# Performance work log

Hardware: AMD Instinct MI355X
Metric: run time of the kernel (lower is better)

Reference implementation:

```python
import jax, jax.numpy as jnp
import numpy as np


def gcn_conv(x, W, b, edge_index, n_nodes):
    """PyG GCNConv: symmetric-normalized aggregation with self-loops.
    out[j] = sum_{(i->j)} deg(i)^-1/2 deg(j)^-1/2 * (x @ W)[i] + b
    """
    xl = x @ W  # [N, H]
    loop = jnp.arange(n_nodes)
    src = jnp.concatenate([edge_index[0], loop])
    dst = jnp.concatenate([edge_index[1], loop])
    deg = jax.ops.segment_sum(jnp.ones_like(dst, dtype=xl.dtype), dst, num_segments=n_nodes)
    dinv = jax.lax.rsqrt(deg)  # deg >= 1 due to self-loops
    norm = dinv[src] * dinv[dst]  # [E+N]
    msg = xl[src] * norm[:, None]  # [E+N, H]
    return jax.ops.segment_sum(msg, dst, num_segments=n_nodes) + b


def reference(x, edge_index_I, edge_index_D, edge_label_index, W_conv, b_conv, W1, b1, W2, b2):
    n = x.shape[0]
    # encode: shared conv over both graphs, relu, sum (dropout off: eval mode)
    h_I = jax.nn.relu(gcn_conv(x, W_conv, b_conv, edge_index_I, n))
    h_D = jax.nn.relu(gcn_conv(x, W_conv, b_conv, edge_index_D, n))
    z = h_I + h_D  # [N, H]
    # decode: gather endpoints, concat [zi, zj, |zi-zj|], small MLP -> scalar per pair
    zi = z[edge_label_index[0]]  # [P, H]
    zj = z[edge_label_index[1]]  # [P, H]
    pair = jnp.concatenate([zi, zj, jnp.abs(zi - zj)], axis=1)  # [P, 3H]
    hdn = jax.nn.relu(pair @ W1 + b1)
    return jnp.squeeze(hdn @ W2 + b2, axis=-1)  # [P]


def setup_inputs() -> dict:
    key = jax.random.key(0)
    ks = jax.random.split(key, 8)
    N, F, H, E, P = 50000, 256, 128, 800000, 500000
    return {
        "x": jax.random.normal(ks[0], (N, F), dtype=jnp.float32),
        "edge_index_I": jax.random.randint(ks[1], (2, E), 0, N, dtype=jnp.int64),
        "edge_index_D": jax.random.randint(ks[2], (2, E), 0, N, dtype=jnp.int64),
        "edge_label_index": jax.random.randint(ks[3], (2, P), 0, N, dtype=jnp.int64),
        "W_conv": jax.random.normal(ks[4], (F, H), dtype=jnp.float32) * (1.0 / np.sqrt(F)),
        "b_conv": jnp.zeros((H,), dtype=jnp.float32),
        "W1": jax.random.normal(ks[5], (3 * H, H), dtype=jnp.float32) * (1.0 / np.sqrt(3 * H)),
        "b1": jnp.zeros((H,), dtype=jnp.float32),
        "W2": jax.random.normal(ks[6], (H, 1), dtype=jnp.float32) * (1.0 / np.sqrt(H)),
        "b2": jnp.zeros((1,), dtype=jnp.float32),
    }
```

## Files before the change

### kernel.cpp

```cpp
#include <hip/hip_runtime.h>

typedef short short8 __attribute__((ext_vector_type(8)));
typedef float f32x4 __attribute__((ext_vector_type(4)));
typedef float f32x16 __attribute__((ext_vector_type(16)));
typedef unsigned short ushort_t;
typedef unsigned int uint_t;

#define HD __device__ __forceinline__

HD ushort_t f2bf(float f) {
    uint_t u = __float_as_uint(f);
    uint_t r = (u + 0x7fffu + ((u >> 16) & 1u)) >> 16;
    return (ushort_t)r;
}
HD float bf2f(ushort_t h) { return __uint_as_float(((uint_t)h) << 16); }
HD float readlane_f(float v, int l) {
    return __int_as_float(__builtin_amdgcn_readlane(__float_as_int(v), l));
}

__global__ __launch_bounds__(256) void gemm_mfma_hilo_bf16(
    const float* __restrict__ A, const ushort_t* __restrict__ Bth,
    const ushort_t* __restrict__ Btl, ushort_t* __restrict__ C,
    int M, int K, int Ntot) {
    __shared__ ushort_t Ah[128][72], Al[128][72], Bh[128][72], Bl[128][72];
    int tid = threadIdx.x;
    int lane = tid & 63, w = tid >> 6;
    int row0 = blockIdx.x * 128;
    int col0 = blockIdx.y * 128;
    int cl = lane & 31, hi = lane >> 5;
    f32x16 acc[4] = {};
    for (int k0 = 0; k0 < K; k0 += 64) {
        for (int e = tid; e < 4096; e += 256) {
            int r = e >> 5, k2 = e & 31;
            int gr = row0 + r;
            float2 v = {0.f, 0.f};
            if (gr < M) v = *(const float2*)&A[(long)gr * K + k0 + k2 * 2];
            ushort_t h0 = f2bf(v.x); ushort_t l0 = f2bf(v.x - bf2f(h0));
            ushort_t h1 = f2bf(v.y); ushort_t l1 = f2bf(v.y - bf2f(h1));
            *(uint_t*)&Ah[r][k2 * 2] = (uint_t)h0 | ((uint_t)h1 << 16);
            *(uint_t*)&Al[r][k2 * 2] = (uint_t)l0 | ((uint_t)l1 << 16);
        }
        for (int e = tid; e < 4096; e += 256) {
            int n = e >> 5, k2 = e & 31;
            const uint_t* ph = (const uint_t*)&Bth[(long)(col0 + n) * K + k0];
            const uint_t* pl = (const uint_t*)&Btl[(long)(col0 + n) * K + k0];
            *(uint_t*)&Bh[n][k2 * 2] = ph[k2];
            *(uint_t*)&Bl[n][k2 * 2] = pl[k2];
        }
        __syncthreads();
        int arow = w * 32 + cl;
#pragma unroll
        for (int kk = 0; kk < 4; ++kk) {
            int koff = kk * 16 + hi * 8;
            short8 a_h = *(const short8*)&Ah[arow][koff];
            short8 a_l = *(const short8*)&Al[arow][koff];
#pragma unroll
            for (int nf = 0; nf < 4; ++nf) {
                int bcol = nf * 32 + cl;
                short8 b_h = *(const short8*)&Bh[bcol][koff];
                short8 b_l = *(const short8*)&Bl[bcol][koff];
                acc[nf] = __builtin_amdgcn_mfma_f32_32x32x16_bf16(a_h, b_h, acc[nf], 0, 0, 0);
                acc[nf] = __builtin_amdgcn_mfma_f32_32x32x16_bf16(a_l, b_h, acc[nf], 0, 0, 0);
                acc[nf] = __builtin_amdgcn_mfma_f32_32x32x16_bf16(a_h, b_l, acc[nf], 0, 0, 0);
            }
        }
        __syncthreads();
    }
#pragma unroll
    for (int nf = 0; nf < 4; ++nf) {
#pragma unroll
        for (int reg = 0; reg < 16; ++reg) {
            int crow = (reg & 3) + 8 * (reg >> 2) + 4 * hi + w * 32;
            int gr = row0 + crow;
            if (gr < M) C[(long)gr * Ntot + col0 + nf * 32 + cl] = f2bf(acc[nf][reg]);
        }
    }
}

__global__ void prep_bt_conv(const float* __restrict__ Wc, ushort_t* bh, ushort_t* bl) {
    int idx = blockIdx.x * 256 + threadIdx.x;
    if (idx >= 128 * 256) return;
    int n = idx >> 8, k = idx & 255;
    float v = Wc[k * 128 + n];
    ushort_t h = f2bf(v);
    bh[idx] = h;
    bl[idx] = f2bf(v - bf2f(h));
}

__global__ void prep_w1frag(const float* __restrict__ W1, ushort_t* __restrict__ w1f) {
    int idx = blockIdx.x * 256 + threadIdx.x;
    if (idx >= 3 * 16384) return;
    int m = idx >> 14;
    int rem = idx & 16383;
    int f = rem >> 9, l = (rem >> 3) & 63, e = rem & 7;
    int t = f >> 2, kk = f & 3;
    int col = 16 * t + (l & 15);
    int k = kk * 32 + (l >> 4) * 8 + e;
    w1f[idx] = f2bf(W1[(m * 128 + k) * 128 + col]);
}

__global__ void zero_ints(int* p, int n) {
    int i = blockIdx.x * 256 + threadIdx.x;
    if (i < n) p[i] = 0;
}

__global__ void count_deg(const int* __restrict__ dstI, const int* __restrict__ dstD,
                          int* cnt, int N, int E) {
    int e = blockIdx.x * 256 + threadIdx.x;
    if (e < E) {
        atomicAdd(&cnt[dstI[e]], 1);
        atomicAdd(&cnt[N + dstD[e]], 1);
    }
}

__global__ void scan_partial(const int* __restrict__ cnt, int* partials, int n2) {
    __shared__ int sdata[256];
    int i = blockIdx.x * 256 + threadIdx.x;
    sdata[threadIdx.x] = (i < n2) ? cnt[i] : 0;
    __syncthreads();
    for (int s = 128; s > 0; s >>= 1) {
        if (threadIdx.x < s) sdata[threadIdx.x] += sdata[threadIdx.x + s];
        __syncthreads();
    }
    if (threadIdx.x == 0) partials[blockIdx.x] = sdata[0];
}

__global__ void scan_partials_excl2(int* partials, int nb) {
    __shared__ int sd[512];
    int t = threadIdx.x;
    int v = (t < nb) ? partials[t] : 0;
    sd[t] = v;
    __syncthreads();
    for (int s = 1; s < 512; s <<= 1) {
        int u = (t >= s) ? sd[t - s] : 0;
        __syncthreads();
        sd[t] += u;
        __syncthreads();
    }
    if (t < nb) partials[t] = sd[t] - v;
}

__global__ void scan_final(const int* __restrict__ cnt, const int* __restrict__ partials,
                           int* off, int* cur, float* dI, float* dD, int N, int n2) {
    __shared__ int sdata[256];
    int i = blockIdx.x * 256 + threadIdx.x;
    int v = (i < n2) ? cnt[i] : 0;
    sdata[threadIdx.x] = v;
    __syncthreads();
    for (int s = 1; s < 256; s <<= 1) {
        int t = (threadIdx.x >= s) ? sdata[threadIdx.x - s] : 0;
        __syncthreads();
        sdata[threadIdx.x] += t;
        __syncthreads();
    }
    int excl = sdata[threadIdx.x] - v + partials[blockIdx.x];
    if (i < n2) {
        off[i] = excl; cur[i] = excl;
        float dv = rsqrtf((float)(v + 1));
        if (i < N) dI[i] = dv; else dD[i - N] = dv;
    }
}

__global__ void fill_csr(const int* __restrict__ srcI, const int* __restrict__ dstI,
                         const int* __restrict__ srcD, const int* __restrict__ dstD,
                         const float* __restrict__ dI, const float* __restrict__ dD,
                         int* cur, int2* __restrict__ edg, int N, int E) {
    int e = blockIdx.x * 256 + threadIdx.x;
    if (e < E) {
        int s = srcI[e], d = dstI[e];
        int pos = atomicAdd(&cur[d], 1);
        edg[pos] = make_int2(s, __float_as_int(dI[s] * dI[d]));
        s = srcD[e]; d = dstD[e];
        pos = atomicAdd(&cur[N + d], 1);
        edg[pos] = make_int2(s, __float_as_int(dD[s] * dD[d]));
    }
}

__global__ __launch_bounds__(256) void gather_combine3(
    const ushort_t* __restrict__ xlb,
    const int* __restrict__ off, const int2* __restrict__ edg,
    const float* __restrict__ dI, const float* __restrict__ dD,
    const float* __restrict__ bconv,
    ushort_t* __restrict__ zh, int N, int E2) {
    int d = blockIdx.x * 4 + (threadIdx.x >> 6);
    int lane = threadIdx.x & 63;
    if (d >= N) return;
    const uint_t* x2 = (const uint_t*)xlb;
    uint_t xdp = x2[(long)d * 64 + lane];
    float xdx = bf2f((ushort_t)(xdp & 0xffff)), xdy = bf2f((ushort_t)(xdp >> 16));
    float aI = dI[d], aD = dD[d];
    float2 accI, accD;
    {
        float c = aI * aI;
        accI.x = c * xdx; accI.y = c * xdy;
        c = aD * aD;
        accD.x = c * xdx; accD.y = c * xdy;
    }
#pragma unroll
    for (int g = 0; g < 2; ++g) {
        int s0 = (g == 0) ? off[d] : off[N + d];
        int e0 = (g == 0) ? off[d + 1] : ((d == N - 1) ? E2 : off[N + d + 1]);
        float2 a0 = {0.f, 0.f}, a1 = {0.f, 0.f}, a2 = {0.f, 0.f}, a3 = {0.f, 0.f};
        float2 a4 = {0.f, 0.f}, a5 = {0.f, 0.f}, a6 = {0.f, 0.f}, a7 = {0.f, 0.f};
        for (int k0 = s0; k0 < e0; k0 += 64) {
            int nk = min(64, e0 - k0);
            int2 ec = (lane < nk) ? edg[k0 + lane] : make_int2(0, 0);
            int sv = ec.x;
            float cv = __int_as_float(ec.y);
            for (int k = 0; k < nk; k += 8) {
                int i0 = __builtin_amdgcn_readlane(sv, k);
                int i1 = __builtin_amdgcn_readlane(sv, k + 1);
                int i2 = __builtin_amdgcn_readlane(sv, k + 2);
                int i3 = __builtin_amdgcn_readlane(sv, k + 3);
                int i4 = __builtin_amdgcn_readlane(sv, k + 4);
                int i5 = __builtin_amdgcn_readlane(sv, k + 5);
                int i6 = __builtin_amdgcn_readlane(sv, k + 6);
                int i7 = __builtin_amdgcn_readlane(sv, k + 7);
                uint_t p0 = x2[(long)i0 * 64 + lane];
                uint_t p1 = x2[(long)i1 * 64 + lane];
                uint_t p2 = x2[(long)i2 * 64 + lane];
                uint_t p3 = x2[(long)i3 * 64 + lane];
                uint_t p4 = x2[(long)i4 * 64 + lane];
                uint_t p5 = x2[(long)i5 * 64 + lane];
                uint_t p6 = x2[(long)i6 * 64 + lane];
                uint_t p7 = x2[(long)i7 * 64 + lane];
                float c0 = readlane_f(cv, k);
                float c1 = readlane_f(cv, k + 1);
                float c2 = readlane_f(cv, k + 2);
                float c3 = readlane_f(cv, k + 3);
                float c4 = readlane_f(cv, k + 4);
                float c5 = readlane_f(cv, k + 5);
                float c6 = readlane_f(cv, k + 6);
                float c7 = readlane_f(cv, k + 7);
                a0.x = fmaf(c0, bf2f((ushort_t)(p0 & 0xffff)), a0.x);
                a0.y = fmaf(c0, bf2f((ushort_t)(p0 >> 16)), a0.y);
                a1.x = fmaf(c1, bf2f((ushort_t)(p1 & 0xffff)), a1.x);
                a1.y = fmaf(c1, bf2f((ushort_t)(p1 >> 16)), a1.y);
                a2.x = fmaf(c2, bf2f((ushort_t)(p2 & 0xffff)), a2.x);
                a2.y = fmaf(c2, bf2f((ushort_t)(p2 >> 16)), a2.y);
                a3.x = fmaf(c3, bf2f((ushort_t)(p3 & 0xffff)), a3.x);
                a3.y = fmaf(c3, bf2f((ushort_t)(p3 >> 16)), a3.y);
                a4.x = fmaf(c4, bf2f((ushort_t)(p4 & 0xffff)), a4.x);
                a4.y = fmaf(c4, bf2f((ushort_t)(p4 >> 16)), a4.y);
                a5.x = fmaf(c5, bf2f((ushort_t)(p5 & 0xffff)), a5.x);
                a5.y = fmaf(c5, bf2f((ushort_t)(p5 >> 16)), a5.y);
                a6.x = fmaf(c6, bf2f((ushort_t)(p6 & 0xffff)), a6.x);
                a6.y = fmaf(c6, bf2f((ushort_t)(p6 >> 16)), a6.y);
                a7.x = fmaf(c7, bf2f((ushort_t)(p7 & 0xffff)), a7.x);
                a7.y = fmaf(c7, bf2f((ushort_t)(p7 >> 16)), a7.y);
            }
        }
        float sx = ((a0.x + a1.x) + (a2.x + a3.x)) + ((a4.x + a5.x) + (a6.x + a7.x));
        float sy = ((a0.y + a1.y) + (a2.y + a3.y)) + ((a4.y + a5.y) + (a6.y + a7.y));
        if (g == 0) { accI.x += sx; accI.y += sy; }
        else        { accD.x += sx; accD.y += sy; }
    }
    float2 b = ((const float2*)bconv)[lane];
    float rx = fmaxf(accI.x + b.x, 0.f) + fmaxf(accD.x + b.x, 0.f);
    float ry = fmaxf(accI.y + b.y, 0.f) + fmaxf(accD.y + b.y, 0.f);
    ushort_t hx = f2bf(rx), hy = f2bf(ry);
    ((uint_t*)zh)[(long)d * 64 + lane] = (uint_t)hx | ((uint_t)hy << 16);
}

__global__ __launch_bounds__(512) void decode_mfma7(
    const ushort_t* __restrict__ zh,
    const int* __restrict__ ei, const int* __restrict__ ej,
    const ushort_t* __restrict__ w1f,
    const float* __restrict__ b1, const float* __restrict__ W2, const float* __restrict__ b2,
    float* __restrict__ out, int P) {
    __shared__ ushort_t Wlds[2][16384];
    int tid = threadIdx.x;
    int lane = tid & 63, w = tid >> 6;
    int r = lane & 15, q = lane >> 4;
    int base = blockIdx.x * 128 + w * 16;
    bool active = base < P;
    int iv = 0, jv = 0;
    if (active && lane < 16) {
        int p = min(base + lane, P - 1);
        iv = ei[p]; jv = ej[p];
    }
    int myi = __shfl(iv, r, 64);
    int myj = __shfl(jv, r, 64);

    short8 zih[4], zjh[4];
    if (active) {
        const ushort_t* pih = zh + (long)myi * 128 + q * 8;
        const ushort_t* pjh = zh + (long)myj * 128 + q * 8;
#pragma unroll
        for (int kk = 0; kk < 4; ++kk) {
            zih[kk] = *(const short8*)(pih + kk * 32);
            zjh[kk] = *(const short8*)(pjh + kk * 32);
        }
    }

    {
        const float4* s4 = (const float4*)w1f;
        float4* d4 = (float4*)Wlds[0];
#pragma unroll
        for (int t2 = 0; t2 < 4; ++t2) d4[t2 * 512 + tid] = s4[t2 * 512 + tid];
    }
    __syncthreads();

    f32x4 acc[8] = {};

#define COMPUTE(buf, AH)                                                        \
    if (active) {                                                               \
        _Pragma("unroll")                                                       \
        for (int t = 0; t < 8; ++t) {                                           \
            _Pragma("unroll")                                                   \
            for (int kk = 0; kk < 4; ++kk) {                                    \
                short8 bh = *(const short8*)&Wlds[buf][(t * 4 + kk) * 512 + lane * 8]; \
                acc[t] = __builtin_amdgcn_mfma_f32_16x16x32_bf16(AH[kk], bh, acc[t], 0, 0, 0); \
            }                                                                   \
        }                                                                       \
    }

    float4 pre[4];
    {
        const float4* s4 = (const float4*)(w1f + 16384);
#pragma unroll
        for (int t2 = 0; t2 < 4; ++t2) pre[t2] = s4[t2 * 512 + tid];
    }
    COMPUTE(0, zih);
    {
        float4* d4 = (float4*)Wlds[1];
#pragma unroll
        for (int t2 = 0; t2 < 4; ++t2) d4[t2 * 512 + tid] = pre[t2];
    }
    __syncthreads();

    {
        const float4* s4 = (const float4*)(w1f + 2 * 16384);
#pragma unroll
        for (int t2 = 0; t2 < 4; ++t2) pre[t2] = s4[t2 * 512 + tid];
    }
    COMPUTE(1, zjh);
    if (active) {
#pragma unroll
        for (int kk = 0; kk < 4; ++kk) {
#pragma unroll
            for (int e = 0; e < 8; ++e) {
                float a = bf2f((ushort_t)zih[kk][e]);
                float b = bf2f((ushort_t)zjh[kk][e]);
                zih[kk][e] = (short)f2bf(fabsf(a - b));
            }
        }
    }
    {
        float4* d4 = (float4*)Wlds[0];
#pragma unroll
        for (int t2 = 0; t2 < 4; ++t2) d4[t2 * 512 + tid] = pre[t2];
    }
    __syncthreads();

    COMPUTE(0, zih);
#undef COMPUTE

    if (!active) return;
    float b2v = b2[0];
    float b1c[8], w2c[8];
#pragma unroll
    for (int t = 0; t < 8; ++t) {
        int col = 16 * t + r;
        b1c[t] = b1[col];
        w2c[t] = W2[col];
    }
#pragma unroll
    for (int r2 = 0; r2 < 4; ++r2) {
        int row = q * 4 + r2;
        float s = 0.f;
#pragma unroll
        for (int t = 0; t < 8; ++t) {
            float h = acc[t][r2] + b1c[t];
            s += fmaxf(h, 0.f) * w2c[t];
        }
        s += __shfl_xor(s, 1, 64);
        s += __shfl_xor(s, 2, 64);
        s += __shfl_xor(s, 4, 64);
        s += __shfl_xor(s, 8, 64);
        int gp = base + row;
        if (r == 0 && gp < P) out[gp] = s + b2v;
    }
}

extern "C" void kernel_launch(void* const* d_in, const int* in_sizes, int n_in,
                              void* d_out, int out_size, void* d_ws, size_t ws_size,
                              hipStream_t stream) {
    const float* x  = (const float*)d_in[0];
    const int*   eI = (const int*)d_in[1];
    const int*   eD = (const int*)d_in[2];
    const int*   eL = (const int*)d_in[3];
    const float* Wconv = (const float*)d_in[4];
    const float* bconv = (const float*)d_in[5];
    const float* W1 = (const float*)d_in[6];
    const float* b1 = (const float*)d_in[7];
    const float* W2 = (const float*)d_in[8];
    const float* b2 = (const float*)d_in[9];

    int N = in_sizes[0] / 256;
    int E = in_sizes[1] / 2;
    int P = in_sizes[3] / 2;
    long NH = (long)N * 128;

    float* ws = (float*)d_ws;
    ushort_t* xlb = (ushort_t*)ws;
    ushort_t* zh = xlb + NH;
    float* dI = (float*)(zh + NH);
    float* dD = dI + N;
    int* iws = (int*)(dD + N);
    int n2 = 2 * N;
    int* cnt = iws;
    int* off = cnt + n2;
    int* cur = off + n2;
    int nb = (n2 + 255) / 256;
    int* partials = cur + n2;
    int2* edg = (int2*)(partials + ((nb + 63) & ~63));
    ushort_t* w1f = (ushort_t*)(edg + 2 * (long)E);
    ushort_t* btch = w1f + 3 * 16384;
    ushort_t* btcl = btch + 32768;
    float* out = (float*)d_out;

    prep_bt_conv<<<128, 256, 0, stream>>>(Wconv, btch, btcl);
    prep_w1frag<<<192, 256, 0, stream>>>(W1, w1f);

    dim3 gx((N + 127) / 128, 1);
    gemm_mfma_hilo_bf16<<<gx, 256, 0, stream>>>(x, btch, btcl, xlb, N, 256, 128);

    zero_ints<<<(n2 + 255) / 256, 256, 0, stream>>>(cnt, n2);
    count_deg<<<(E + 255) / 256, 256, 0, stream>>>(eI + E, eD + E, cnt, N, E);
    scan_partial<<<nb, 256, 0, stream>>>(cnt, partials, n2);
    scan_partials_excl2<<<1, 512, 0, stream>>>(partials, nb);
    scan_final<<<nb, 256, 0, stream>>>(cnt, partials, off, cur, dI, dD, N, n2);
    fill_csr<<<(E + 255) / 256, 256, 0, stream>>>(eI, eI + E, eD, eD + E, dI, dD,
                                                  cur, edg, N, E);

    gather_combine3<<<(N + 3) / 4, 256, 0, stream>>>(xlb, off, edg, dI, dD,
                                                     bconv, zh, N, 2 * E);

    decode_mfma7<<<(P + 127) / 128, 512, 0, stream>>>(zh, eL, eL + P, w1f,
                                                      b1, W2, b2, out, P);
}
```

Before: 342.1 us.

## Replace direct CSR fill with two-pass coarse-bucket then fine scatter

Replaces the single-pass atomic CSR fill with a two-level bucketed scatter. Edges are first counted into coarse destination bins of 128 nodes, scanned, and scattered into a temporary buffer grouped by bin. A fine pass then places each edge at its final CSR slot. The goal is to localise the atomics and random writes of the fine pass, at the cost of extra kernel launches and an additional full read and write of the edge list.

```diff
diff --git a/kernel.cpp b/kernel.cpp
--- a/kernel.cpp
+++ b/kernel.cpp
@@ -7,6 +7,7 @@
 typedef unsigned int uint_t;
 
 #define HD __device__ __forceinline__
+#define NBSHIFT 7
 
 HD ushort_t f2bf(float f) {
     uint_t u = __float_as_uint(f);
@@ -161,18 +162,64 @@
     }
 }
 
-__global__ void fill_csr(const int* __restrict__ srcI, const int* __restrict__ dstI,
-                         const int* __restrict__ srcD, const int* __restrict__ dstD,
-                         const float* __restrict__ dI, const float* __restrict__ dD,
-                         int* cur, int2* __restrict__ edg, int N, int E) {
+__global__ __launch_bounds__(256) void coarse_count(
+    const int* __restrict__ dstI, const int* __restrict__ dstD,
+    int* __restrict__ ccnt, int N, int E, int NB) {
+    __shared__ int bins[1024];
+    for (int b = threadIdx.x; b < NB; b += 256) bins[b] = 0;
+    __syncthreads();
+    int stride = gridDim.x * 256;
+    for (int e = blockIdx.x * 256 + threadIdx.x; e < E; e += stride) {
+        atomicAdd(&bins[dstI[e] >> NBSHIFT], 1);
+        atomicAdd(&bins[(N + dstD[e]) >> NBSHIFT], 1);
+    }
+    __syncthreads();
+    for (int b = threadIdx.x; b < NB; b += 256) {
+        int v = bins[b];
+        if (v) atomicAdd(&ccnt[b], v);
+    }
+}
+
+__global__ void coarse_scan(const int* __restrict__ ccnt, int* ccur, int NB) {
+    __shared__ int sd[1024];
+    int t = threadIdx.x;
+    int v = (t < NB) ? ccnt[t] : 0;
+    sd[t] = v;
+    __syncthreads();
+    for (int s = 1; s < 1024; s <<= 1) {
+        int u = (t >= s) ? sd[t - s] : 0;
+        __syncthreads();
+        sd[t] += u;
+        __syncthreads();
+    }
+    if (t < NB) ccur[t] = sd[t] - v;
+}
+
+__global__ void coarse_scatter(const int* __restrict__ srcI, const int* __restrict__ dstI,
+                               const int* __restrict__ srcD, const int* __restrict__ dstD,
+                               int* ccur, int2* __restrict__ tmp, int N, int E) {
     int e = blockIdx.x * 256 + threadIdx.x;
     if (e < E) {
         int s = srcI[e], d = dstI[e];
+        int pos = atomicAdd(&ccur[d >> NBSHIFT], 1);
+        tmp[pos] = make_int2(s, d);
+        s = srcD[e]; d = N + dstD[e];
+        pos = atomicAdd(&ccur[d >> NBSHIFT], 1);
+        tmp[pos] = make_int2(s, d);
+    }
+}
+
+__global__ __launch_bounds__(256) void fine_scatter(
+    const int2* __restrict__ tmp, int* cur,
+    const float* __restrict__ dI, const float* __restrict__ dD,
+    int2* __restrict__ edg, int N, int E2) {
+    int stride = gridDim.x * 256;
+    for (int e = blockIdx.x * 256 + threadIdx.x; e < E2; e += stride) {
+        int2 t = tmp[e];
+        int s = t.x, d = t.y;
         int pos = atomicAdd(&cur[d], 1);
-        edg[pos] = make_int2(s, __float_as_int(dI[s] * dI[d]));
-        s = srcD[e]; d = dstD[e];
-        pos = atomicAdd(&cur[N + d], 1);
-        edg[pos] = make_int2(s, __float_as_int(dD[s] * dD[d]));
+        float coef = (d < N) ? dI[s] * dI[d] : dD[s] * dD[d - N];
+        edg[pos] = make_int2(s, __float_as_int(coef));
     }
 }
 
@@ -401,6 +448,8 @@
     int E = in_sizes[1] / 2;
     int P = in_sizes[3] / 2;
     long NH = (long)N * 128;
+    int n2 = 2 * N;
+    int NB = (n2 + 127) >> NBSHIFT;
 
     float* ws = (float*)d_ws;
     ushort_t* xlb = (ushort_t*)ws;
@@ -408,14 +457,16 @@
     float* dI = (float*)(zh + NH);
     float* dD = dI + N;
     int* iws = (int*)(dD + N);
-    int n2 = 2 * N;
     int* cnt = iws;
     int* off = cnt + n2;
     int* cur = off + n2;
     int nb = (n2 + 255) / 256;
     int* partials = cur + n2;
-    int2* edg = (int2*)(partials + ((nb + 63) & ~63));
-    ushort_t* w1f = (ushort_t*)(edg + 2 * (long)E);
+    int* ccnt = partials + ((nb + 63) & ~63);
+    int* ccur = ccnt + 1024;
+    int2* edg = (int2*)(ccur + 1024);
+    int2* tmp = edg + 2 * (long)E;
+    ushort_t* w1f = (ushort_t*)(tmp + 2 * (long)E);
     ushort_t* btch = w1f + 3 * 16384;
     ushort_t* btcl = btch + 32768;
     float* out = (float*)d_out;
@@ -427,12 +478,17 @@
     gemm_mfma_hilo_bf16<<<gx, 256, 0, stream>>>(x, btch, btcl, xlb, N, 256, 128);
 
     zero_ints<<<(n2 + 255) / 256, 256, 0, stream>>>(cnt, n2);
+    zero_ints<<<4, 256, 0, stream>>>(ccnt, 1024);
     count_deg<<<(E + 255) / 256, 256, 0, stream>>>(eI + E, eD + E, cnt, N, E);
     scan_partial<<<nb, 256, 0, stream>>>(cnt, partials, n2);
     scan_partials_excl2<<<1, 512, 0, stream>>>(partials, nb);
     scan_final<<<nb, 256, 0, stream>>>(cnt, partials, off, cur, dI, dD, N, n2);
-    fill_csr<<<(E + 255) / 256, 256, 0, stream>>>(eI, eI + E, eD, eD + E, dI, dD,
-                                                  cur, edg, N, E);
+
+    coarse_count<<<256, 256, 0, stream>>>(eI + E, eD + E, ccnt, N, E, NB);
+    coarse_scan<<<1, 1024, 0, stream>>>(ccnt, ccur, NB);
+    coarse_scatter<<<(E + 255) / 256, 256, 0, stream>>>(eI, eI + E, eD, eD + E,
+                                                        ccur, tmp, N, E);
+    fine_scatter<<<1024, 256, 0, stream>>>(tmp, cur, dI, dD, edg, N, 2 * E);
 
     gather_combine3<<<(N + 3) / 4, 256, 0, stream>>>(xlb, off, edg, dI, dD,
                                                      bconv, zh, N, 2 * E);
```

Result: slower. 737.4 us (+115.5%).
